# Performance work log

Measured on AMD Instinct MI355X. Metric: run time of the kernel, lower is better.

Reference implementation:

```python
import jax, jax.numpy as jnp
import numpy as np

MIN_WEIGHT = 0.0
MAX_WEIGHT = 500.0


def setup_inputs() -> dict:
    key = jax.random.key(0)
    k1, k2, k3 = jax.random.split(key, 3)
    B, P = 131072, 64   # groundings, predicates
    C, L = 128, 3       # clauses, literals per clause
    ground_atoms = jax.random.normal(k1, (B, P), dtype=jnp.float32)
    # learned clause weights, initial_clause_weight = 0.5
    clause_weights = 0.5 * jnp.ones((C,), dtype=jnp.float32)
    # which predicate each literal refers to
    literal_idx = jax.random.randint(k2, (C, L), 0, P, dtype=jnp.int64)
    # 0 -> negated literal (sign -1), 1 -> positive literal (sign +1)
    sign_bits = jax.random.randint(k3, (C, L), 0, 2, dtype=jnp.int32)
    return {
        "ground_atoms": ground_atoms,
        "clause_weights": clause_weights,
        "literal_idx": literal_idx,
        "sign_bits": sign_bits,
    }


def reference(ground_atoms, clause_weights, literal_idx, sign_bits):
    """Vectorized KnowledgeEnhancer forward.

    Per clause (GodelBoostConormApprox):
      literals = signs * ground_atoms[:, idx]
      delta    = signs * clamp(w) * softmax(literals)
    Then concat all clause deltas and scatter_add into predicate space.
    """
    B, P = ground_atoms.shape
    C, L = literal_idx.shape
    signs = (2 * sign_bits - 1).astype(ground_atoms.dtype)  # [C, L] in {-1,+1}
    gathered = ground_atoms[:, literal_idx]                 # [B, C, L] gather
    literals = signs[None, :, :] * gathered                 # signed pre-activations
    w = jnp.clip(clause_weights, MIN_WEIGHT, MAX_WEIGHT)    # [C]
    delta = signs[None, :, :] * w[None, :, None] * jax.nn.softmax(literals, axis=-1)
    # concat over clauses (dim=1 in the torch code) then scatter_add over predicates
    delta_flat = delta.reshape(B, C * L)
    idx_flat = literal_idx.reshape(C * L)
    out = jax.ops.segment_sum(delta_flat.T, idx_flat, num_segments=P)  # [P, B]
    return out.T  # [B, P]
```

## Files before the change

### kernel.cpp

```cpp
#include <hip/hip_runtime.h>
#include <stdint.h>

typedef unsigned int  u32;
typedef unsigned short u16;

#define B_ROWS 131072
#define P_PRED 64
#define C_CLS  128
#define NPAIR  384
#define CAP    32
#define RPB    64
#define TPB    512
#define LSTR   129
#define LOG2E  1.4426950408889634f

#if __has_builtin(__builtin_amdgcn_exp2f)
#define EXP2F(x) __builtin_amdgcn_exp2f(x)
#else
#define EXP2F(x) exp2f(x)
#endif

#if __has_builtin(__builtin_amdgcn_rcpf)
#define RCPF(x) __builtin_amdgcn_rcpf(x)
#else
#define RCPF(x) (1.0f / (x))
#endif

__device__ __forceinline__ float bf16_to_f(u16 u) {
    return __uint_as_float(((u32)u) << 16);
}
__device__ __forceinline__ u16 f_to_bf16(float f) {
    u32 u = __float_as_uint(f);
    u += 0x7FFFu + ((u >> 16) & 1u);
    return (u16)(u >> 16);
}

__global__ void ke_prep(const u32* __restrict__ lidx_w,
                        const u32* __restrict__ sb_w,
                        const u32* __restrict__ w_w,
                        u32* __restrict__ recs,
                        int* __restrict__ cnts,
                        u32* __restrict__ flags) {
    __shared__ int scnt[P_PRED];
    __shared__ int sidx[NPAIR];
    __shared__ int ssb[NPAIR];
    __shared__ int det[3];
    const int t = threadIdx.x;
    if (t < P_PRED) scnt[t] = 0;
    if (t < 3) det[t] = 1;
    __syncthreads();
    if (t < NPAIR / 2) {
        if (lidx_w[2 * t + 1] != 0u) det[0] = 0;
        if (sb_w[2 * t + 1]   != 0u) det[1] = 0;
    }
    if (t == 0 && (w_w[0] & 0xFFFFu) == 0u) det[2] = 0;
    __syncthreads();
    if (t < NPAIR) {
        sidx[t] = (int)(det[0] ? lidx_w[2 * t] : lidx_w[t]);
        ssb[t]  = (int)(det[1] ? sb_w[2 * t]   : sb_w[t]);
    }
    __syncthreads();
    if (t < NPAIR) {
        const int c = t / 3;
        const int l = t - c * 3;
        const int base = c * 3;
        const int o1 = base + (l == 0 ? 1 : 0);
        const int o2 = base + (l == 2 ? 1 : 2);
        const int p = sidx[t];
        const int slot = atomicAdd(&scnt[p], 1);
        float wraw = det[2] ? bf16_to_f((u16)(w_w[c / 2] >> ((c & 1) * 16)))
                            : __uint_as_float(w_w[c]);
        float wc = fminf(fmaxf(wraw, 0.0f), 500.0f);
        if (slot < CAP) {
            u32* r = recs + (p * CAP + slot) * 4;
            r[0] = (u32)(2 * sidx[t]  + (ssb[t]  ? 0 : 1));
            r[1] = (u32)(2 * sidx[o1] + (ssb[o1] ? 0 : 1));
            r[2] = (u32)(2 * sidx[o2] + (ssb[o2] ? 0 : 1));
            r[3] = __float_as_uint(ssb[t] ? wc : -wc);
        }
    }
    __syncthreads();
    if (t < P_PRED) cnts[t] = min(scnt[t], CAP);
    if (t == 0) flags[0] = (u32)det[2];
}

__global__ __launch_bounds__(TPB, 8)
void ke_main(const void* __restrict__ atoms_v,
             const u32* __restrict__ recs_u,
             const int* __restrict__ cnts,
             const u32* __restrict__ flags,
             void* __restrict__ out_v) {
    __shared__ float E[RPB * LSTR];
    const int tid = threadIdx.x;
    const int row = tid & (RPB - 1);
    const int grp = __builtin_amdgcn_readfirstlane(tid >> 6);
    const int rowBase = blockIdx.x * RPB;
    const bool bf16m = (flags[0] != 0u);

    {
        const int srow = tid >> 3;
        const int c0 = (tid & 7) * 8;
        float* dst = &E[srow * LSTR + 2 * c0];
        if (bf16m) {
            const u16* g = (const u16*)atoms_v + (size_t)(rowBase + srow) * P_PRED + c0;
            uint4 v = *(const uint4*)g;
            u32 w[4] = {v.x, v.y, v.z, v.w};
#pragma unroll
            for (int j = 0; j < 4; ++j) {
                float x0 = __uint_as_float(w[j] << 16) * LOG2E;
                float x1 = __uint_as_float(w[j] & 0xFFFF0000u) * LOG2E;
                dst[4 * j + 0] = EXP2F(x0);
                dst[4 * j + 1] = EXP2F(-x0);
                dst[4 * j + 2] = EXP2F(x1);
                dst[4 * j + 3] = EXP2F(-x1);
            }
        } else {
            const float* g = (const float*)atoms_v + (size_t)(rowBase + srow) * P_PRED + c0;
            float4 v0 = *(const float4*)g;
            float4 v1 = *(const float4*)(g + 4);
            float xs[8] = {v0.x, v0.y, v0.z, v0.w, v1.x, v1.y, v1.z, v1.w};
#pragma unroll
            for (int j = 0; j < 8; ++j) {
                float x = xs[j] * LOG2E;
                dst[2 * j + 0] = EXP2F(x);
                dst[2 * j + 1] = EXP2F(-x);
            }
        }
    }
    __syncthreads();

    const float* Lrow = &E[row * LSTR];

    float acc[8];
#pragma unroll
    for (int pp = 0; pp < 8; ++pp) {
        const int p = grp * 8 + pp;
        const int n = min(cnts[p], CAP);
        const u32* rp = recs_u + p * CAP * 4;
        float a = 0.0f;
        for (int e = 0; e < n; ++e) {
            const u32* r = rp + e * 4;
            float ss = Lrow[r[0]];
            float s1 = Lrow[r[1]];
            float s2 = Lrow[r[2]];
            float sw = __uint_as_float(r[3]);
            a += sw * ss * RCPF(ss + s1 + s2);
        }
        acc[pp] = a;
    }

    if (bf16m) {
        u16* op = (u16*)out_v + (size_t)(rowBase + row) * P_PRED + grp * 8;
        uint4 o;
        o.x = (u32)f_to_bf16(acc[0]) | ((u32)f_to_bf16(acc[1]) << 16);
        o.y = (u32)f_to_bf16(acc[2]) | ((u32)f_to_bf16(acc[3]) << 16);
        o.z = (u32)f_to_bf16(acc[4]) | ((u32)f_to_bf16(acc[5]) << 16);
        o.w = (u32)f_to_bf16(acc[6]) | ((u32)f_to_bf16(acc[7]) << 16);
        *(uint4*)op = o;
    } else {
        float* op = (float*)out_v + (size_t)(rowBase + row) * P_PRED + grp * 8;
        *(float4*)(op)     = make_float4(acc[0], acc[1], acc[2], acc[3]);
        *(float4*)(op + 4) = make_float4(acc[4], acc[5], acc[6], acc[7]);
    }
}

extern "C" void kernel_launch(void* const* d_in, const int* in_sizes, int n_in,
                              void* d_out, int out_size, void* d_ws, size_t ws_size,
                              hipStream_t stream) {
    const u32* clause_weights = (const u32*)d_in[1];
    const u32* literal_idx    = (const u32*)d_in[2];
    const u32* sign_bits      = (const u32*)d_in[3];

    u32* recs  = (u32*)d_ws;
    int* cnts  = (int*)((char*)d_ws + P_PRED * CAP * 16);
    u32* flags = (u32*)((char*)d_ws + P_PRED * CAP * 16 + 256);

    ke_prep<<<1, NPAIR, 0, stream>>>(literal_idx, sign_bits, clause_weights,
                                     recs, cnts, flags);
    ke_main<<<B_ROWS / RPB, TPB, 0, stream>>>(d_in[0], recs, cnts, flags, d_out);
}
```

Measured before the change: 106.9 us.

## Transpose LDS exp table, pack clause records into wave registers, two rows per lane

The LDS table becomes predicate-major and holds only exp(x). exp(-x) is recovered with a reciprocal, which halves LDS size and the number of exp evaluations. Clause records are packed into 8-byte entries per predicate group, loaded once into VGPRs and broadcast with readlane, which removes the scalar/global record loads from the inner loop. Each lane now handles two rows with float2 LDS reads, and blocks cover 128 rows. The cost is extra reciprocals per literal, a per-group cap of 128 records that can drop clauses, and more register pressure.

```diff
diff --git a/kernel.cpp b/kernel.cpp
--- a/kernel.cpp
+++ b/kernel.cpp
@@ -9,9 +9,9 @@
 #define C_CLS  128
 #define NPAIR  384
 #define CAP    32
-#define RPB    64
+#define RPB    128
 #define TPB    512
-#define LSTR   129
+#define GCAP   128
 #define LOG2E  1.4426950408889634f
 
 #if __has_builtin(__builtin_amdgcn_exp2f)
@@ -38,10 +38,12 @@
 __global__ void ke_prep(const u32* __restrict__ lidx_w,
                         const u32* __restrict__ sb_w,
                         const u32* __restrict__ w_w,
-                        u32* __restrict__ recs,
-                        int* __restrict__ cnts,
+                        uint2* __restrict__ stream,
+                        u32* __restrict__ cnt8w,
                         u32* __restrict__ flags) {
     __shared__ int scnt[P_PRED];
+    __shared__ u32 recPk[P_PRED][CAP];
+    __shared__ float recW[P_PRED][CAP];
     __shared__ int sidx[NPAIR];
     __shared__ int ssb[NPAIR];
     __shared__ int det[3];
@@ -72,110 +74,155 @@
                             : __uint_as_float(w_w[c]);
         float wc = fminf(fmaxf(wraw, 0.0f), 500.0f);
         if (slot < CAP) {
-            u32* r = recs + (p * CAP + slot) * 4;
-            r[0] = (u32)(2 * sidx[t]  + (ssb[t]  ? 0 : 1));
-            r[1] = (u32)(2 * sidx[o1] + (ssb[o1] ? 0 : 1));
-            r[2] = (u32)(2 * sidx[o2] + (ssb[o2] ? 0 : 1));
-            r[3] = __float_as_uint(ssb[t] ? wc : -wc);
-        }
-    }
-    __syncthreads();
-    if (t < P_PRED) cnts[t] = min(scnt[t], CAP);
+            u32 s1 = 2u * (u32)sidx[o1] + (ssb[o1] ? 0u : 1u);
+            u32 s2 = 2u * (u32)sidx[o2] + (ssb[o2] ? 0u : 1u);
+            recPk[p][slot] = (ssb[t] ? 0u : 1u) | (s1 << 8) | (s2 << 16);
+            recW[p][slot]  = ssb[t] ? wc : -wc;
+        }
+    }
+    __syncthreads();
+    if (t < P_PRED) {
+        const int p = t;
+        const int g = p >> 3;
+        const int n = min(scnt[p], CAP);
+        int off = 0;
+        for (int pb = g * 8; pb < p; ++pb) off += min(scnt[pb], CAP);
+        int ncl = 0;
+        for (int j = 0; j < n; ++j) {
+            if (off + j < GCAP) {
+                stream[g * GCAP + off + j] =
+                    make_uint2(recPk[p][j], __float_as_uint(recW[p][j]));
+                ++ncl;
+            }
+        }
+        ((unsigned char*)cnt8w)[p] = (unsigned char)ncl;
+    }
     if (t == 0) flags[0] = (u32)det[2];
 }
 
 __global__ __launch_bounds__(TPB, 8)
 void ke_main(const void* __restrict__ atoms_v,
-             const u32* __restrict__ recs_u,
-             const int* __restrict__ cnts,
+             const uint2* __restrict__ stream,
+             const u32* __restrict__ cnt8w,
              const u32* __restrict__ flags,
              void* __restrict__ out_v) {
-    __shared__ float E[RPB * LSTR];
+    __shared__ float E[P_PRED * RPB];
     const int tid = threadIdx.x;
-    const int row = tid & (RPB - 1);
-    const int grp = __builtin_amdgcn_readfirstlane(tid >> 6);
+    const int lane = tid & 63;
+    const int g = __builtin_amdgcn_readfirstlane(tid >> 6);
     const int rowBase = blockIdx.x * RPB;
     const bool bf16m = (flags[0] != 0u);
 
     {
-        const int srow = tid >> 3;
-        const int c0 = (tid & 7) * 8;
-        float* dst = &E[srow * LSTR + 2 * c0];
+        const int r = tid >> 2;
+        const int c0 = (tid & 3) * 16;
         if (bf16m) {
-            const u16* g = (const u16*)atoms_v + (size_t)(rowBase + srow) * P_PRED + c0;
-            uint4 v = *(const uint4*)g;
-            u32 w[4] = {v.x, v.y, v.z, v.w};
-#pragma unroll
-            for (int j = 0; j < 4; ++j) {
-                float x0 = __uint_as_float(w[j] << 16) * LOG2E;
-                float x1 = __uint_as_float(w[j] & 0xFFFF0000u) * LOG2E;
-                dst[4 * j + 0] = EXP2F(x0);
-                dst[4 * j + 1] = EXP2F(-x0);
-                dst[4 * j + 2] = EXP2F(x1);
-                dst[4 * j + 3] = EXP2F(-x1);
-            }
-        } else {
-            const float* g = (const float*)atoms_v + (size_t)(rowBase + srow) * P_PRED + c0;
-            float4 v0 = *(const float4*)g;
-            float4 v1 = *(const float4*)(g + 4);
-            float xs[8] = {v0.x, v0.y, v0.z, v0.w, v1.x, v1.y, v1.z, v1.w};
+            const u16* gp = (const u16*)atoms_v + (size_t)(rowBase + r) * P_PRED + c0;
+            uint4 v0 = *(const uint4*)gp;
+            uint4 v1 = *(const uint4*)(gp + 8);
+            u32 w[8] = {v0.x, v0.y, v0.z, v0.w, v1.x, v1.y, v1.z, v1.w};
 #pragma unroll
             for (int j = 0; j < 8; ++j) {
-                float x = xs[j] * LOG2E;
-                dst[2 * j + 0] = EXP2F(x);
-                dst[2 * j + 1] = EXP2F(-x);
-            }
-        }
-    }
-    __syncthreads();
-
-    const float* Lrow = &E[row * LSTR];
-
-    float acc[8];
+                float xlo = __uint_as_float(w[j] << 16) * LOG2E;
+                float xhi = __uint_as_float(w[j] & 0xFFFF0000u) * LOG2E;
+                E[(c0 + 2 * j)     * RPB + r] = EXP2F(xlo);
+                E[(c0 + 2 * j + 1) * RPB + r] = EXP2F(xhi);
+            }
+        } else {
+            const float* gp = (const float*)atoms_v + (size_t)(rowBase + r) * P_PRED + c0;
+#pragma unroll
+            for (int j4 = 0; j4 < 4; ++j4) {
+                float4 v = *(const float4*)(gp + 4 * j4);
+                E[(c0 + 4 * j4 + 0) * RPB + r] = EXP2F(v.x * LOG2E);
+                E[(c0 + 4 * j4 + 1) * RPB + r] = EXP2F(v.y * LOG2E);
+                E[(c0 + 4 * j4 + 2) * RPB + r] = EXP2F(v.z * LOG2E);
+                E[(c0 + 4 * j4 + 3) * RPB + r] = EXP2F(v.w * LOG2E);
+            }
+        }
+    }
+
+    uint2 rA = stream[g * GCAP + lane];
+    uint2 rB = stream[g * GCAP + 64 + lane];
+    const u32 cntLo = cnt8w[g * 2];
+    const u32 cntHi = cnt8w[g * 2 + 1];
+
+    __syncthreads();
+
+    const int q2 = lane * 2;
+    float2 acc[8];
+    int j = 0;
 #pragma unroll
     for (int pp = 0; pp < 8; ++pp) {
-        const int p = grp * 8 + pp;
-        const int n = min(cnts[p], CAP);
-        const u32* rp = recs_u + p * CAP * 4;
-        float a = 0.0f;
-        for (int e = 0; e < n; ++e) {
-            const u32* r = rp + e * 4;
-            float ss = Lrow[r[0]];
-            float s1 = Lrow[r[1]];
-            float s2 = Lrow[r[2]];
-            float sw = __uint_as_float(r[3]);
-            a += sw * ss * RCPF(ss + s1 + s2);
+        const int p = g * 8 + pp;
+        float2 ep = *(const float2*)&E[p * RPB + q2];
+        float2 epn;
+        epn.x = RCPF(ep.x);
+        epn.y = RCPF(ep.y);
+        const int n = (int)((pp < 4 ? (cntLo >> (8 * pp))
+                                    : (cntHi >> (8 * (pp - 4)))) & 255u);
+        float2 a = make_float2(0.0f, 0.0f);
+        for (int e = 0; e < n; ++e, ++j) {
+            u32 pk, swb;
+            if (j < 64) {
+                pk  = (u32)__builtin_amdgcn_readlane((int)rA.x, j);
+                swb = (u32)__builtin_amdgcn_readlane((int)rA.y, j);
+            } else {
+                pk  = (u32)__builtin_amdgcn_readlane((int)rB.x, j - 64);
+                swb = (u32)__builtin_amdgcn_readlane((int)rB.y, j - 64);
+            }
+            const float sw = __uint_as_float(swb);
+            const u32 o1 = (pk >> 8) & 255u;
+            const u32 o2 = (pk >> 16) & 255u;
+            float2 s1 = *(const float2*)&E[(int)(o1 >> 1) * RPB + q2];
+            float2 s2 = *(const float2*)&E[(int)(o2 >> 1) * RPB + q2];
+            if (o1 & 1u) { s1.x = RCPF(s1.x); s1.y = RCPF(s1.y); }
+            if (o2 & 1u) { s2.x = RCPF(s2.x); s2.y = RCPF(s2.y); }
+            const float2 ss = (pk & 1u) ? epn : ep;
+            float tx = RCPF(ss.x + s1.x + s2.x);
+            float ty = RCPF(ss.y + s1.y + s2.y);
+            a.x = fmaf(sw * ss.x, tx, a.x);
+            a.y = fmaf(sw * ss.y, ty, a.y);
         }
         acc[pp] = a;
     }
 
     if (bf16m) {
-        u16* op = (u16*)out_v + (size_t)(rowBase + row) * P_PRED + grp * 8;
-        uint4 o;
-        o.x = (u32)f_to_bf16(acc[0]) | ((u32)f_to_bf16(acc[1]) << 16);
-        o.y = (u32)f_to_bf16(acc[2]) | ((u32)f_to_bf16(acc[3]) << 16);
-        o.z = (u32)f_to_bf16(acc[4]) | ((u32)f_to_bf16(acc[5]) << 16);
-        o.w = (u32)f_to_bf16(acc[6]) | ((u32)f_to_bf16(acc[7]) << 16);
-        *(uint4*)op = o;
+        u16* op0 = (u16*)out_v + (size_t)(rowBase + q2) * P_PRED + g * 8;
+        u16* op1 = op0 + P_PRED;
+        uint4 o0, o1v;
+        o0.x  = (u32)f_to_bf16(acc[0].x) | ((u32)f_to_bf16(acc[1].x) << 16);
+        o0.y  = (u32)f_to_bf16(acc[2].x) | ((u32)f_to_bf16(acc[3].x) << 16);
+        o0.z  = (u32)f_to_bf16(acc[4].x) | ((u32)f_to_bf16(acc[5].x) << 16);
+        o0.w  = (u32)f_to_bf16(acc[6].x) | ((u32)f_to_bf16(acc[7].x) << 16);
+        o1v.x = (u32)f_to_bf16(acc[0].y) | ((u32)f_to_bf16(acc[1].y) << 16);
+        o1v.y = (u32)f_to_bf16(acc[2].y) | ((u32)f_to_bf16(acc[3].y) << 16);
+        o1v.z = (u32)f_to_bf16(acc[4].y) | ((u32)f_to_bf16(acc[5].y) << 16);
+        o1v.w = (u32)f_to_bf16(acc[6].y) | ((u32)f_to_bf16(acc[7].y) << 16);
+        *(uint4*)op0 = o0;
+        *(uint4*)op1 = o1v;
     } else {
-        float* op = (float*)out_v + (size_t)(rowBase + row) * P_PRED + grp * 8;
-        *(float4*)(op)     = make_float4(acc[0], acc[1], acc[2], acc[3]);
-        *(float4*)(op + 4) = make_float4(acc[4], acc[5], acc[6], acc[7]);
+        float* op0 = (float*)out_v + (size_t)(rowBase + q2) * P_PRED + g * 8;
+        float* op1 = op0 + P_PRED;
+        *(float4*)(op0)     = make_float4(acc[0].x, acc[1].x, acc[2].x, acc[3].x);
+        *(float4*)(op0 + 4) = make_float4(acc[4].x, acc[5].x, acc[6].x, acc[7].x);
+        *(float4*)(op1)     = make_float4(acc[0].y, acc[1].y, acc[2].y, acc[3].y);
+        *(float4*)(op1 + 4) = make_float4(acc[4].y, acc[5].y, acc[6].y, acc[7].y);
     }
 }
 
 extern "C" void kernel_launch(void* const* d_in, const int* in_sizes, int n_in,
                               void* d_out, int out_size, void* d_ws, size_t ws_size,
-                              hipStream_t stream) {
+                              hipStream_t stream_h) {
     const u32* clause_weights = (const u32*)d_in[1];
     const u32* literal_idx    = (const u32*)d_in[2];
     const u32* sign_bits      = (const u32*)d_in[3];
 
-    u32* recs  = (u32*)d_ws;
-    int* cnts  = (int*)((char*)d_ws + P_PRED * CAP * 16);
-    u32* flags = (u32*)((char*)d_ws + P_PRED * CAP * 16 + 256);
-
-    ke_prep<<<1, NPAIR, 0, stream>>>(literal_idx, sign_bits, clause_weights,
-                                     recs, cnts, flags);
-    ke_main<<<B_ROWS / RPB, TPB, 0, stream>>>(d_in[0], recs, cnts, flags, d_out);
-}
+    uint2* stream = (uint2*)d_ws;
+    u32*   cnt8w  = (u32*)((char*)d_ws + 8 * GCAP * 8);
+    u32*   flags  = (u32*)((char*)d_ws + 8 * GCAP * 8 + 64);
+
+    ke_prep<<<1, NPAIR, 0, stream_h>>>(literal_idx, sign_bits, clause_weights,
+                                       stream, cnt8w, flags);
+    ke_main<<<B_ROWS / RPB, TPB, 0, stream_h>>>(d_in[0], stream, cnt8w, flags,
+                                                d_out);
+}
```

Measured after the change: 112.2 us. 1.05x slower.
